# Kernel tuning notes

Hardware: AMD Instinct MI355X
Metric: run time of the kernel (lower is better)

The kernel has to match this reference:

```python
import jax, jax.numpy as jnp
import numpy as np

B, S, D, H = 2, 2048, 1024, 16
HD = D // H                 # head_dim = 64
BLOCK = 16                  # _DEFAULT_BLOCK_SIZE
NB = S // BLOCK             # max_blocks_per_seq = 128
WINDOW = 512
NEG = jnp.float32(-1e30)


def setup_inputs() -> dict:
    key = jax.random.key(0)
    ks = jax.random.split(key, 5)
    x = jax.random.normal(ks[0], (B, S, D), jnp.float32)
    scale = D ** -0.5
    wq = jax.random.normal(ks[1], (D, D), jnp.float32) * scale
    wk = jax.random.normal(ks[2], (D, D), jnp.float32) * scale
    wv = jax.random.normal(ks[3], (D, D), jnp.float32) * scale
    wo = jax.random.normal(ks[4], (D, D), jnp.float32) * scale
    # sequential paged layout (matches the module's synthesized-cache fallback)
    block_tables = jnp.arange(B * NB, dtype=jnp.int32).reshape(B, NB)
    slot_mapping = jnp.arange(B * S, dtype=jnp.int32)
    context_lens = jnp.full((B,), S, dtype=jnp.int32)
    return {"x": x, "wq": wq, "wk": wk, "wv": wv, "wo": wo,
            "block_tables": block_tables, "slot_mapping": slot_mapping,
            "context_lens": context_lens, "window_size": WINDOW}


def reference(x, wq, wk, wv, wo, block_tables, slot_mapping, context_lens, window_size):
    b, s, d = x.shape
    # Q/K/V projections (nn.Linear, bias=False: y = x @ W^T)
    q = (x @ wq.T).reshape(b, s, H, HD)
    k = (x @ wk.T).reshape(b, s, H, HD)
    v = (x @ wv.T).reshape(b, s, H, HD)

    # ---- memopt_C.write_cache: scatter K/V into the physical slot pool ----
    num_slots = b * s
    key_cache = jnp.zeros((num_slots, H, HD), x.dtype).at[slot_mapping].set(k.reshape(-1, H, HD))
    value_cache = jnp.zeros((num_slots, H, HD), x.dtype).at[slot_mapping].set(v.reshape(-1, H, HD))

    # ---- dynamic_sparse_attention: read KV through block_tables ----
    t = jnp.arange(s)
    # physical slot of logical token t of sequence b: block_tables[b, t//BLOCK]*BLOCK + t%BLOCK
    slots = block_tables[:, t // BLOCK].astype(jnp.int32) * BLOCK + (t % BLOCK)[None, :].astype(jnp.int32)  # [B,S]
    kc = key_cache[slots]    # [B,S,H,HD]
    vc = value_cache[slots]  # [B,S,H,HD]

    scores = jnp.einsum('bqhd,bkhd->bhqk', q, kc) * (HD ** -0.5)  # [B,H,S,S]
    qpos = t[:, None]
    kpos = t[None, :]
    # causal + window-limited visibility (window_size tokens of history)
    vis = (kpos <= qpos) & (qpos - kpos < window_size)            # [S,S]
    ctx = t[None, :] < context_lens[:, None]                       # [B,S]
    mask = vis[None, None, :, :] & ctx[:, None, None, :]
    scores = jnp.where(mask, scores, NEG)
    attn = jax.nn.softmax(scores, axis=-1)
    out = jnp.einsum('bhqk,bkhd->bqhd', attn, vc).reshape(b, s, d)
    return out @ wo.T
```

## Files before the change

kernel.cpp:

```cpp
#include <hip/hip_runtime.h>

typedef __attribute__((ext_vector_type(4))) float  f32x4;
typedef __attribute__((ext_vector_type(8))) short  bf16x8;

typedef __attribute__((address_space(3))) void lds_void_t;
typedef __attribute__((address_space(1))) void g_void_t;

#define S_LEN  2048
#define DMODEL 1024
#define NHEAD  16
#define HDIM   64
#define NBLK   128
#define BATCH  2
#define KT     64
#define VP     72

__device__ __forceinline__ short f2bf(float f) {
  union { float f; unsigned u; } v; v.f = f;
  unsigned r = v.u + 0x7fffu + ((v.u >> 16) & 1u);
  return (short)(r >> 16);
}

__global__ __launch_bounds__(256) void cvt_all_kernel(
    const float* __restrict__ x,  const float* __restrict__ wq,
    const float* __restrict__ wk, const float* __restrict__ wv,
    const float* __restrict__ wo,
    short* __restrict__ xb,  short* __restrict__ wqb,
    short* __restrict__ wkb, short* __restrict__ wvb,
    short* __restrict__ wob) {
  const long i = ((long)blockIdx.x * 256 + threadIdx.x) * 8;
  const float* s; short* d; long off;
  if (i < 4194304L)      { s = x;  d = xb;  off = i; }
  else if (i < 5242880L) { s = wq; d = wqb; off = i - 4194304L; }
  else if (i < 6291456L) { s = wk; d = wkb; off = i - 5242880L; }
  else if (i < 7340032L) { s = wv; d = wvb; off = i - 6291456L; }
  else                   { s = wo; d = wob; off = i - 7340032L; }
  f32x4 a = *(const f32x4*)(s + off);
  f32x4 b = *(const f32x4*)(s + off + 4);
  bf16x8 o;
  o[0]=f2bf(a[0]); o[1]=f2bf(a[1]); o[2]=f2bf(a[2]); o[3]=f2bf(a[3]);
  o[4]=f2bf(b[0]); o[5]=f2bf(b[1]); o[6]=f2bf(b[2]); o[7]=f2bf(b[3]);
  *(bf16x8*)(d + off) = o;
}

__global__ __launch_bounds__(512, 2) void gemm8_kernel(
    const short* __restrict__ A,
    const short* __restrict__ W0, const short* __restrict__ W1, const short* __restrict__ W2,
    const int* __restrict__ slot_map,
    short* __restrict__ qbuf, short* __restrict__ kcache, short* __restrict__ vcache)
{
  extern __shared__ short smem[];

  const int m0 = blockIdx.x * 256;
  const int n0 = blockIdx.y * 192;
  const short* Ag = A + (size_t)m0 * DMODEL;

  const int tid  = threadIdx.x;
  const int wave = tid >> 6, lane = tid & 63;
  const int l15 = lane & 15, lg = lane >> 4;
  const int wr = wave >> 2, wc = wave & 3;
  const int swz = l15 & 7;

  short* const A0s = smem;
  short* const B0s = smem + 16384;
  short* const A1s = smem + 28672;
  short* const B1s = smem + 45056;

  f32x4 acc[8][3];
#pragma unroll
  for (int m = 0; m < 8; m++)
#pragma unroll
    for (int n = 0; n < 3; n++) acc[m][n] = (f32x4)0.f;

#define STAGE_A(DST, K0, P) {                                                              \
    const int gidx = (P) * 512 + tid;                                                      \
    const int r = gidx >> 3;                                                               \
    const int cs = (gidx & 7) ^ (r & 7);                                                   \
    __builtin_amdgcn_global_load_lds((g_void_t*)(Ag + (size_t)r * DMODEL + (K0) + cs * 8), \
        (lds_void_t*)((DST) + ((P) * 512 + wave * 64) * 8), 16, 0, 0); }

#define STAGE_B(DST, K0, P) {                                                              \
    const int gidx = (P) * 512 + tid;                                                      \
    const int r = gidx >> 3;                                                               \
    const int grow = n0 + r;                                                               \
    const short* wb = (grow < 1024) ? W0 : (grow < 2048) ? W1 : W2;                        \
    const int cs = (gidx & 7) ^ (r & 7);                                                   \
    __builtin_amdgcn_global_load_lds((g_void_t*)(wb + (size_t)(grow & 1023) * DMODEL + (K0) + cs * 8), \
        (lds_void_t*)((DST) + ((P) * 512 + wave * 64) * 8), 16, 0, 0); }

#define PHASE_BAR() do {                                        \
    asm volatile("" ::: "memory");                              \
    __builtin_amdgcn_s_barrier();                               \
    asm volatile("" ::: "memory");                              \
  } while (0)

#define PHASE_READ_A(BUF, Q)                                                               \
    _Pragma("unroll") for (int mi = 0; mi < 2; ++mi) {                                     \
      const int row = wr * 128 + ((Q) * 2 + mi) * 16 + l15;                                \
      _Pragma("unroll") for (int ks = 0; ks < 2; ++ks)                                     \
        af[mi][ks] = *(const bf16x8*)((BUF) + row * 64 + (((ks * 4 + lg) ^ swz) << 3)); }

#define PHASE_MFMA(Q)                                                                      \
    __builtin_amdgcn_s_setprio(1);                                                         \
    _Pragma("unroll") for (int mi = 0; mi < 2; ++mi)                                       \
    _Pragma("unroll") for (int nt = 0; nt < 3; ++nt)                                       \
    _Pragma("unroll") for (int ks = 0; ks < 2; ++ks)                                       \
      acc[(Q) * 2 + mi][nt] = __builtin_amdgcn_mfma_f32_16x16x32_bf16(                     \
          af[mi][ks], bfr[nt][ks], acc[(Q) * 2 + mi][nt], 0, 0, 0);                        \
    __builtin_amdgcn_s_setprio(0);

  STAGE_B(B0s, 0, 0); STAGE_B(B0s, 0, 1); STAGE_B(B0s, 0, 2);
  STAGE_A(A0s, 0, 0); STAGE_A(A0s, 0, 2); STAGE_A(A0s, 0, 1); STAGE_A(A0s, 0, 3);
  asm volatile("s_waitcnt vmcnt(0)" ::: "memory");
  __builtin_amdgcn_s_barrier();
  asm volatile("" ::: "memory");

  const int NT = DMODEL / 64;
  for (int t = 0; t < NT; ++t) {
    const bool stg = (t + 1 < NT);
    short* const Ac = (t & 1) ? A1s : A0s;
    short* const Bc = (t & 1) ? B1s : B0s;
    short* const An = (t & 1) ? A0s : A1s;
    short* const Bn = (t & 1) ? B0s : B1s;
    const int kn = (t + 1) * 64;

    bf16x8 af[2][2], bfr[3][2];

#pragma unroll
    for (int nt = 0; nt < 3; ++nt) {
      const int row = wc * 48 + nt * 16 + l15;
#pragma unroll
      for (int ks = 0; ks < 2; ++ks)
        bfr[nt][ks] = *(const bf16x8*)(Bc + row * 64 + (((ks * 4 + lg) ^ swz) << 3));
    }
    PHASE_READ_A(Ac, 0);
    if (stg) { STAGE_B(Bn, kn, 0); STAGE_B(Bn, kn, 1); STAGE_B(Bn, kn, 2); }
    PHASE_BAR();
    PHASE_MFMA(0);
    PHASE_BAR();

    PHASE_READ_A(Ac, 1);
    if (stg) { STAGE_A(An, kn, 0); STAGE_A(An, kn, 2); }
    PHASE_BAR();
    PHASE_MFMA(1);
    if (stg) { asm volatile("s_waitcnt vmcnt(6)" ::: "memory"); }
    else     { asm volatile("s_waitcnt vmcnt(1)" ::: "memory"); }
    PHASE_BAR();

    PHASE_READ_A(Ac, 2);
    if (stg) { STAGE_A(An, kn, 1); }
    PHASE_BAR();
    PHASE_MFMA(2);
    if (stg) { asm volatile("s_waitcnt vmcnt(6)" ::: "memory"); }
    else     { asm volatile("s_waitcnt vmcnt(0)" ::: "memory"); }
    PHASE_BAR();

    PHASE_READ_A(Ac, 3);
    if (stg) { STAGE_A(An, kn, 3); }
    PHASE_BAR();
    PHASE_MFMA(3);
    asm volatile("s_waitcnt vmcnt(2)" ::: "memory");
    PHASE_BAR();
  }
#undef STAGE_A
#undef STAGE_B
#undef PHASE_BAR
#undef PHASE_READ_A
#undef PHASE_MFMA

#pragma unroll
  for (int mf = 0; mf < 8; ++mf) {
    const int rowb = m0 + wr * 128 + mf * 16 + lg * 4;
#pragma unroll
    for (int r4 = 0; r4 < 4; ++r4) {
      const int row = rowb + r4;
      const int slot = slot_map[row];
#pragma unroll
      for (int nt = 0; nt < 3; ++nt) {
        const int col = n0 + wc * 48 + nt * 16 + l15;
        const short bv = f2bf(acc[mf][nt][r4]);
        if (col < DMODEL)
          qbuf[(size_t)row * DMODEL + col] = bv;
        else if (col < 2 * DMODEL)
          kcache[(size_t)slot * DMODEL + (col - DMODEL)] = bv;
        else
          vcache[(size_t)slot * DMODEL + (col - 2 * DMODEL)] = bv;
      }
    }
  }
}

__global__ __launch_bounds__(256) void gemm1_kernel(
    const short* __restrict__ A, const short* __restrict__ W,
    float* __restrict__ outf)
{
  __shared__ short As[2][64 * 64];
  __shared__ short Bs[2][128 * 64];

  const int m0 = blockIdx.x * 64;
  const int n0 = blockIdx.y * 128;
  const short* Ag = A + (size_t)m0 * DMODEL;
  const short* Bg = W + (size_t)n0 * DMODEL;

  const int tid = threadIdx.x;
  const int wave = tid >> 6, lane = tid & 63;
  const int l15 = lane & 15, lg = lane >> 4;
  const int swz = l15 & 7;

  f32x4 acc[4][2];
#pragma unroll
  for (int m = 0; m < 4; m++)
#pragma unroll
    for (int n = 0; n < 2; n++) acc[m][n] = (f32x4)0.f;

#define STG1(BUF, K0) {                                                                    \
    _Pragma("unroll") for (int p = 0; p < 2; ++p) {                                        \
      const int u = p * 256 + tid; const int r = u >> 3; const int cs = (u & 7) ^ (r & 7); \
      __builtin_amdgcn_global_load_lds((g_void_t*)(Ag + (size_t)r * DMODEL + (K0) + cs * 8), \
          (lds_void_t*)(As[BUF] + (p * 256 + wave * 64) * 8), 16, 0, 0); }                 \
    _Pragma("unroll") for (int p = 0; p < 4; ++p) {                                        \
      const int u = p * 256 + tid; const int r = u >> 3; const int cs = (u & 7) ^ (r & 7); \
      __builtin_amdgcn_global_load_lds((g_void_t*)(Bg + (size_t)r * DMODEL + (K0) + cs * 8), \
          (lds_void_t*)(Bs[BUF] + (p * 256 + wave * 64) * 8), 16, 0, 0); } }

  STG1(0, 0);
  asm volatile("s_waitcnt vmcnt(0)" ::: "memory");
  __builtin_amdgcn_s_barrier();
  asm volatile("" ::: "memory");

  for (int t = 0; t < 16; ++t) {
    const int cur = t & 1;
    if (t + 1 < 16) {
      STG1(cur ^ 1, (t + 1) * 64);
      asm volatile("s_waitcnt vmcnt(6)" ::: "memory");
    } else {
      asm volatile("s_waitcnt vmcnt(0)" ::: "memory");
    }
    asm volatile("" ::: "memory");
    __builtin_amdgcn_s_barrier();
    asm volatile("" ::: "memory");

    bf16x8 af[4][2], bfr[2][2];
#pragma unroll
    for (int m4 = 0; m4 < 4; ++m4) {
      const int row = m4 * 16 + l15;
#pragma unroll
      for (int ks = 0; ks < 2; ++ks)
        af[m4][ks] = *(const bf16x8*)(As[cur] + row * 64 + (((ks * 4 + lg) ^ swz) << 3));
    }
#pragma unroll
    for (int n2 = 0; n2 < 2; ++n2) {
      const int row = wave * 32 + n2 * 16 + l15;
#pragma unroll
      for (int ks = 0; ks < 2; ++ks)
        bfr[n2][ks] = *(const bf16x8*)(Bs[cur] + row * 64 + (((ks * 4 + lg) ^ swz) << 3));
    }
    __builtin_amdgcn_s_setprio(1);
#pragma unroll
    for (int m4 = 0; m4 < 4; ++m4)
#pragma unroll
      for (int n2 = 0; n2 < 2; ++n2)
#pragma unroll
        for (int ks = 0; ks < 2; ++ks)
          acc[m4][n2] = __builtin_amdgcn_mfma_f32_16x16x32_bf16(af[m4][ks], bfr[n2][ks], acc[m4][n2], 0, 0, 0);
    __builtin_amdgcn_s_setprio(0);

    asm volatile("" ::: "memory");
    __builtin_amdgcn_s_barrier();
    asm volatile("" ::: "memory");
  }
#undef STG1

#pragma unroll
  for (int m4 = 0; m4 < 4; ++m4) {
    const int rowb = m0 + m4 * 16 + lg * 4;
#pragma unroll
    for (int n2 = 0; n2 < 2; ++n2) {
      const int col = n0 + wave * 32 + n2 * 16 + l15;
#pragma unroll
      for (int r4 = 0; r4 < 4; ++r4)
        outf[(size_t)(rowb + r4) * DMODEL + col] = acc[m4][n2][r4];
    }
  }
}

__global__ __launch_bounds__(512, 4) void attn_kernel(
    const short* __restrict__ qbuf,
    const short* __restrict__ kcache, const short* __restrict__ vcache,
    const int* __restrict__ block_tables, const int* __restrict__ context_lens,
    const int* __restrict__ window_size,
    short* __restrict__ attn_out)
{
  __shared__ short Ks[KT * 64];
  __shared__ short Vt[HDIM * VP];
  __shared__ short Pb[8 * 16 * VP];

  const int b = blockIdx.z, h = blockIdx.y;
  const int bx = (b & 1) ? ((int)gridDim.x - 1 - (int)blockIdx.x) : (int)blockIdx.x;
  const int q0 = bx * 128;
  const int ctx = context_lens[b];
  const int ws  = window_size[0];
  const int* bt = block_tables + b * NBLK;

  const int tid  = threadIdx.x;
  const int wave = tid >> 6, lane = tid & 63;
  const int l15 = lane & 15, lg = lane >> 4;
  const int qw = q0 + wave * 16;

  const short* qp = qbuf + ((size_t)(b * S_LEN + qw + l15)) * DMODEL + h * HDIM;
  const bf16x8 qf0 = *(const bf16x8*)(qp + lg * 8);
  const bf16x8 qf1 = *(const bf16x8*)(qp + 32 + lg * 8);

  f32x4 oacc[4];
  float lrow[4];
#pragma unroll
  for (int i = 0; i < 4; i++) { oacc[i] = (f32x4)0.f; lrow[i] = 0.f; }

  int kstart = q0 - ws + 1; if (kstart < 0) kstart = 0; kstart &= ~(KT - 1);
  int kend = q0 + 128; if (kend > ctx) kend = ctx;

  const int kr = tid >> 3;
  const int dc = (tid & 7) << 3;
  const float rscale = 0.125f;
  const float FM = 12.f;
  short* pw = Pb + wave * (16 * VP);
  const int swz = (l15 & 7) << 4;

  bf16x8 kreg = (bf16x8)0, vreg = (bf16x8)0;
  {
    const int key = kstart + kr;
    if (key < ctx) {
      const int slot = bt[key >> 4] * 16 + (key & 15);
      kreg = *(const bf16x8*)(kcache + (size_t)slot * DMODEL + h * HDIM + dc);
      vreg = *(const bf16x8*)(vcache + (size_t)slot * DMODEL + h * HDIM + dc);
    }
  }

  for (int kt = kstart; kt < kend; kt += KT) {
    __syncthreads();
    *(bf16x8*)((char*)Ks + kr * 128 + ((dc * 2) ^ ((kr & 7) << 4))) = kreg;
    const int vcol = (kr + dc) & 63;
#pragma unroll
    for (int j = 0; j < 8; j++) Vt[(dc + j) * VP + vcol] = vreg[j];
    kreg = (bf16x8)0; vreg = (bf16x8)0;
    if (kt + KT < kend) {
      const int key = kt + KT + kr;
      if (key < ctx) {
        const int slot = bt[key >> 4] * 16 + (key & 15);
        kreg = *(const bf16x8*)(kcache + (size_t)slot * DMODEL + h * HDIM + dc);
        vreg = *(const bf16x8*)(vcache + (size_t)slot * DMODEL + h * HDIM + dc);
      }
    }
    __syncthreads();

    if ((kt > qw + 15) || (kt + (KT - 1) <= qw - ws)) continue;

    f32x4 sacc[4];
#pragma unroll
    for (int cg = 0; cg < 4; cg++) sacc[cg] = (f32x4)0.f;
#pragma unroll
    for (int cg = 0; cg < 4; cg++) {
      const char* kp = (const char*)Ks + (cg * 16 + l15) * 128;
      const bf16x8 k0 = *(const bf16x8*)(kp + ((lg * 16) ^ swz));
      const bf16x8 k1 = *(const bf16x8*)(kp + ((64 + lg * 16) ^ swz));
      sacc[cg] = __builtin_amdgcn_mfma_f32_16x16x32_bf16(qf0, k0, sacc[cg], 0, 0, 0);
      sacc[cg] = __builtin_amdgcn_mfma_f32_16x16x32_bf16(qf1, k1, sacc[cg], 0, 0, 0);
    }

    const bool fullvis = (kt + (KT - 1) <= qw) && (qw + 15 - kt < ws) && (kt + (KT - 1) < ctx);

    if (fullvis) {
#pragma unroll
      for (int r = 0; r < 4; r++) {
        const float e0 = __expf(sacc[0][r] * rscale - FM);
        const float e1 = __expf(sacc[1][r] * rscale - FM);
        const float e2 = __expf(sacc[2][r] * rscale - FM);
        const float e3 = __expf(sacc[3][r] * rscale - FM);
        lrow[r] += (e0 + e1) + (e2 + e3);
        short* pr = pw + (lg * 4 + r) * VP + l15;
        pr[0]  = f2bf(e0); pr[16] = f2bf(e1);
        pr[32] = f2bf(e2); pr[48] = f2bf(e3);
      }
    } else {
#pragma unroll
      for (int r = 0; r < 4; r++) {
        const int qrow = qw + lg * 4 + r;
        const int key0 = kt + l15;
        const bool ok0 = (key0      <= qrow) && (qrow - key0      < ws) && (key0      < ctx);
        const bool ok1 = (key0 + 16 <= qrow) && (qrow - key0 - 16 < ws) && (key0 + 16 < ctx);
        const bool ok2 = (key0 + 32 <= qrow) && (qrow - key0 - 32 < ws) && (key0 + 32 < ctx);
        const bool ok3 = (key0 + 48 <= qrow) && (qrow - key0 - 48 < ws) && (key0 + 48 < ctx);
        const float e0 = ok0 ? __expf(sacc[0][r] * rscale - FM) : 0.f;
        const float e1 = ok1 ? __expf(sacc[1][r] * rscale - FM) : 0.f;
        const float e2 = ok2 ? __expf(sacc[2][r] * rscale - FM) : 0.f;
        const float e3 = ok3 ? __expf(sacc[3][r] * rscale - FM) : 0.f;
        lrow[r] += (e0 + e1) + (e2 + e3);
        short* pr = pw + (lg * 4 + r) * VP + l15;
        pr[0]  = f2bf(e0); pr[16] = f2bf(e1);
        pr[32] = f2bf(e2); pr[48] = f2bf(e3);
      }
    }

    asm volatile("s_waitcnt lgkmcnt(0)" ::: "memory");

#pragma unroll
    for (int kk = 0; kk < 2; kk++) {
      const bf16x8 pa = *(const bf16x8*)(pw + l15 * VP + kk * 32 + lg * 8);
#pragma unroll
      for (int dn = 0; dn < 4; dn++) {
        const int vrow = dn * 16 + l15;
        const int roff = (kk * 32 + lg * 8 + (vrow & ~7)) & 63;
        const bf16x8 vb = *(const bf16x8*)(Vt + vrow * VP + roff);
        oacc[dn] = __builtin_amdgcn_mfma_f32_16x16x32_bf16(pa, vb, oacc[dn], 0, 0, 0);
      }
    }
  }

#pragma unroll
  for (int r = 0; r < 4; r++) {
    float ls = lrow[r];
    ls += __shfl_xor(ls, 1); ls += __shfl_xor(ls, 2);
    ls += __shfl_xor(ls, 4); ls += __shfl_xor(ls, 8);
    const float inv = 1.f / fmaxf(ls, 1e-30f);
    const int row = qw + lg * 4 + r;
    short* op = attn_out + ((size_t)(b * S_LEN + row)) * DMODEL + h * HDIM;
#pragma unroll
    for (int dn = 0; dn < 4; dn++)
      op[dn * 16 + l15] = f2bf(oacc[dn][r] * inv);
  }
}

extern "C" void kernel_launch(void* const* d_in, const int* in_sizes, int n_in,
                              void* d_out, int out_size, void* d_ws, size_t ws_size,
                              hipStream_t stream) {
  const float* x  = (const float*)d_in[0];
  const float* wq = (const float*)d_in[1];
  const float* wk = (const float*)d_in[2];
  const float* wv = (const float*)d_in[3];
  const float* wo = (const float*)d_in[4];
  const int* block_tables = (const int*)d_in[5];
  const int* slot_mapping = (const int*)d_in[6];
  const int* context_lens = (const int*)d_in[7];
  const int* window_size  = (const int*)d_in[8];
  float* out = (float*)d_out;

  char* ws = (char*)d_ws;
  short* xb     = (short*)(ws + (size_t)( 0 << 20));
  short* wqb    = (short*)(ws + (size_t)( 8 << 20));
  short* wkb    = (short*)(ws + (size_t)(10 << 20));
  short* wvb    = (short*)(ws + (size_t)(12 << 20));
  short* wob    = (short*)(ws + (size_t)(14 << 20));
  short* qbuf   = (short*)(ws + (size_t)(16 << 20));
  short* kcache = (short*)(ws + (size_t)(24 << 20));
  short* vcache = (short*)(ws + (size_t)(32 << 20));
  short* abuf   = (short*)(ws + (size_t)(40 << 20));

  static bool gemm8_init = [] {
    hipFuncSetAttribute(reinterpret_cast<const void*>(&gemm8_kernel),
                        hipFuncAttributeMaxDynamicSharedMemorySize, 114688);
    return true;
  }();
  (void)gemm8_init;

  cvt_all_kernel<<<4096, 256, 0, stream>>>(x, wq, wk, wv, wo, xb, wqb, wkb, wvb, wob);

  gemm8_kernel<<<dim3(16, 16), 512, 114688, stream>>>(xb, wqb, wkb, wvb, slot_mapping,
                                                      qbuf, kcache, vcache);

  attn_kernel<<<dim3(S_LEN / 128, NHEAD, BATCH), 512, 0, stream>>>(
      qbuf, kcache, vcache, block_tables, context_lens, window_size, abuf);

  gemm1_kernel<<<dim3(64, 8), 256, 0, stream>>>(abuf, wob, out);
}
```

Baseline: 90.61 us.

## Enlarge output-projection GEMM tile to 128x128 and reshuffle QKV GEMM staging

The output-projection GEMM now computes 128x128 tiles with a 2x2 wave layout, and its double-buffered LDS moves to 64KB of dynamic shared memory. The grid is halved to 256 blocks, which raises per-block operand reuse and cuts global traffic per FLOP. In exchange the GPU is less full and each thread holds more accumulator registers. The QKV GEMM loop also issues all A-stage loads earlier, moving the vmcnt waits so that phase 3 has no staging in it.

```diff
diff --git a/kernel.cpp b/kernel.cpp
--- a/kernel.cpp
+++ b/kernel.cpp
@@ -143,23 +143,21 @@
     if (stg) { STAGE_A(An, kn, 0); STAGE_A(An, kn, 2); }
     PHASE_BAR();
     PHASE_MFMA(1);
-    if (stg) { asm volatile("s_waitcnt vmcnt(6)" ::: "memory"); }
-    else     { asm volatile("s_waitcnt vmcnt(1)" ::: "memory"); }
+    if (stg) { asm volatile("s_waitcnt vmcnt(5)" ::: "memory"); }
+    else     { asm volatile("s_waitcnt vmcnt(0)" ::: "memory"); }
     PHASE_BAR();
 
     PHASE_READ_A(Ac, 2);
-    if (stg) { STAGE_A(An, kn, 1); }
+    if (stg) { STAGE_A(An, kn, 1); STAGE_A(An, kn, 3); }
     PHASE_BAR();
     PHASE_MFMA(2);
-    if (stg) { asm volatile("s_waitcnt vmcnt(6)" ::: "memory"); }
+    PHASE_BAR();
+
+    PHASE_READ_A(Ac, 3);
+    PHASE_BAR();
+    PHASE_MFMA(3);
+    if (stg) { asm volatile("s_waitcnt vmcnt(2)" ::: "memory"); }
     else     { asm volatile("s_waitcnt vmcnt(0)" ::: "memory"); }
-    PHASE_BAR();
-
-    PHASE_READ_A(Ac, 3);
-    if (stg) { STAGE_A(An, kn, 3); }
-    PHASE_BAR();
-    PHASE_MFMA(3);
-    asm volatile("s_waitcnt vmcnt(2)" ::: "memory");
     PHASE_BAR();
   }
 #undef STAGE_A
@@ -190,14 +188,13 @@
   }
 }
 
-__global__ __launch_bounds__(256) void gemm1_kernel(
+__global__ __launch_bounds__(256, 2) void gemm1_kernel(
     const short* __restrict__ A, const short* __restrict__ W,
     float* __restrict__ outf)
 {
-  __shared__ short As[2][64 * 64];
-  __shared__ short Bs[2][128 * 64];
-
-  const int m0 = blockIdx.x * 64;
+  extern __shared__ short smem1[];
+
+  const int m0 = blockIdx.x * 128;
   const int n0 = blockIdx.y * 128;
   const short* Ag = A + (size_t)m0 * DMODEL;
   const short* Bg = W + (size_t)n0 * DMODEL;
@@ -205,34 +202,44 @@
   const int tid = threadIdx.x;
   const int wave = tid >> 6, lane = tid & 63;
   const int l15 = lane & 15, lg = lane >> 4;
+  const int wr = wave >> 1, wc = wave & 1;
   const int swz = l15 & 7;
 
-  f32x4 acc[4][2];
+  short* const As0 = smem1;
+  short* const Bs0 = smem1 + 8192;
+  short* const As1 = smem1 + 16384;
+  short* const Bs1 = smem1 + 24576;
+
+  f32x4 acc[4][4];
 #pragma unroll
   for (int m = 0; m < 4; m++)
 #pragma unroll
-    for (int n = 0; n < 2; n++) acc[m][n] = (f32x4)0.f;
-
-#define STG1(BUF, K0) {                                                                    \
-    _Pragma("unroll") for (int p = 0; p < 2; ++p) {                                        \
+    for (int n = 0; n < 4; n++) acc[m][n] = (f32x4)0.f;
+
+#define STG1(LA, LB, K0) {                                                                 \
+    _Pragma("unroll") for (int p = 0; p < 4; ++p) {                                        \
       const int u = p * 256 + tid; const int r = u >> 3; const int cs = (u & 7) ^ (r & 7); \
       __builtin_amdgcn_global_load_lds((g_void_t*)(Ag + (size_t)r * DMODEL + (K0) + cs * 8), \
-          (lds_void_t*)(As[BUF] + (p * 256 + wave * 64) * 8), 16, 0, 0); }                 \
+          (lds_void_t*)((LA) + (p * 256 + wave * 64) * 8), 16, 0, 0); }                    \
     _Pragma("unroll") for (int p = 0; p < 4; ++p) {                                        \
       const int u = p * 256 + tid; const int r = u >> 3; const int cs = (u & 7) ^ (r & 7); \
       __builtin_amdgcn_global_load_lds((g_void_t*)(Bg + (size_t)r * DMODEL + (K0) + cs * 8), \
-          (lds_void_t*)(Bs[BUF] + (p * 256 + wave * 64) * 8), 16, 0, 0); } }
-
-  STG1(0, 0);
+          (lds_void_t*)((LB) + (p * 256 + wave * 64) * 8), 16, 0, 0); } }
+
+  STG1(As0, Bs0, 0);
   asm volatile("s_waitcnt vmcnt(0)" ::: "memory");
   __builtin_amdgcn_s_barrier();
   asm volatile("" ::: "memory");
 
   for (int t = 0; t < 16; ++t) {
     const int cur = t & 1;
+    short* const Ac = cur ? As1 : As0;
+    short* const Bc = cur ? Bs1 : Bs0;
+    short* const An = cur ? As0 : As1;
+    short* const Bn = cur ? Bs0 : Bs1;
     if (t + 1 < 16) {
-      STG1(cur ^ 1, (t + 1) * 64);
-      asm volatile("s_waitcnt vmcnt(6)" ::: "memory");
+      STG1(An, Bn, (t + 1) * 64);
+      asm volatile("s_waitcnt vmcnt(8)" ::: "memory");
     } else {
       asm volatile("s_waitcnt vmcnt(0)" ::: "memory");
     }
@@ -240,29 +247,29 @@
     __builtin_amdgcn_s_barrier();
     asm volatile("" ::: "memory");
 
-    bf16x8 af[4][2], bfr[2][2];
+    bf16x8 af[4][2], bfr[4][2];
 #pragma unroll
     for (int m4 = 0; m4 < 4; ++m4) {
-      const int row = m4 * 16 + l15;
+      const int row = wr * 64 + m4 * 16 + l15;
 #pragma unroll
       for (int ks = 0; ks < 2; ++ks)
-        af[m4][ks] = *(const bf16x8*)(As[cur] + row * 64 + (((ks * 4 + lg) ^ swz) << 3));
-    }
-#pragma unroll
-    for (int n2 = 0; n2 < 2; ++n2) {
-      const int row = wave * 32 + n2 * 16 + l15;
+        af[m4][ks] = *(const bf16x8*)(Ac + row * 64 + (((ks * 4 + lg) ^ swz) << 3));
+    }
+#pragma unroll
+    for (int n4 = 0; n4 < 4; ++n4) {
+      const int row = wc * 64 + n4 * 16 + l15;
 #pragma unroll
       for (int ks = 0; ks < 2; ++ks)
-        bfr[n2][ks] = *(const bf16x8*)(Bs[cur] + row * 64 + (((ks * 4 + lg) ^ swz) << 3));
+        bfr[n4][ks] = *(const bf16x8*)(Bc + row * 64 + (((ks * 4 + lg) ^ swz) << 3));
     }
     __builtin_amdgcn_s_setprio(1);
 #pragma unroll
     for (int m4 = 0; m4 < 4; ++m4)
 #pragma unroll
-      for (int n2 = 0; n2 < 2; ++n2)
+      for (int n4 = 0; n4 < 4; ++n4)
 #pragma unroll
         for (int ks = 0; ks < 2; ++ks)
-          acc[m4][n2] = __builtin_amdgcn_mfma_f32_16x16x32_bf16(af[m4][ks], bfr[n2][ks], acc[m4][n2], 0, 0, 0);
+          acc[m4][n4] = __builtin_amdgcn_mfma_f32_16x16x32_bf16(af[m4][ks], bfr[n4][ks], acc[m4][n4], 0, 0, 0);
     __builtin_amdgcn_s_setprio(0);
 
     asm volatile("" ::: "memory");
@@ -273,13 +280,13 @@
 
 #pragma unroll
   for (int m4 = 0; m4 < 4; ++m4) {
-    const int rowb = m0 + m4 * 16 + lg * 4;
-#pragma unroll
-    for (int n2 = 0; n2 < 2; ++n2) {
-      const int col = n0 + wave * 32 + n2 * 16 + l15;
+    const int rowb = m0 + wr * 64 + m4 * 16 + lg * 4;
+#pragma unroll
+    for (int n4 = 0; n4 < 4; ++n4) {
+      const int col = n0 + wc * 64 + n4 * 16 + l15;
 #pragma unroll
       for (int r4 = 0; r4 < 4; ++r4)
-        outf[(size_t)(rowb + r4) * DMODEL + col] = acc[m4][n2][r4];
+        outf[(size_t)(rowb + r4) * DMODEL + col] = acc[m4][n4][r4];
     }
   }
 }
@@ -455,12 +462,14 @@
   short* vcache = (short*)(ws + (size_t)(32 << 20));
   short* abuf   = (short*)(ws + (size_t)(40 << 20));
 
-  static bool gemm8_init = [] {
+  static bool ginit = [] {
     hipFuncSetAttribute(reinterpret_cast<const void*>(&gemm8_kernel),
                         hipFuncAttributeMaxDynamicSharedMemorySize, 114688);
+    hipFuncSetAttribute(reinterpret_cast<const void*>(&gemm1_kernel),
+                        hipFuncAttributeMaxDynamicSharedMemorySize, 65536);
     return true;
   }();
-  (void)gemm8_init;
+  (void)ginit;
 
   cvt_all_kernel<<<4096, 256, 0, stream>>>(x, wq, wk, wv, wo, xb, wqb, wkb, wvb, wob);
 
@@ -470,5 +479,5 @@
   attn_kernel<<<dim3(S_LEN / 128, NHEAD, BATCH), 512, 0, stream>>>(
       qbuf, kcache, vcache, block_tables, context_lens, window_size, abuf);
 
-  gemm1_kernel<<<dim3(64, 8), 256, 0, stream>>>(abuf, wob, out);
-}
+  gemm1_kernel<<<dim3(32, 8), 256, 65536, stream>>>(abuf, wob, out);
+}
```

After: 89.82 us. About the same (-0.9%).
